# Kernel tuning notes

Hardware: AMD Instinct MI355X
Metric: run time of the kernel (lower is better)

Reference implementation:

```python
import jax, jax.numpy as jnp
import numpy as np

B, L, D, H, NL, DFF = 32, 64, 256, 8, 2, 2048
S, I, DSEM, DDENSE, DSPARSE = 16, 16, 128, 128, 128


def layer_norm(x, g, b, eps=1e-5):
    m = x.mean(-1, keepdims=True)
    v = ((x - m) ** 2).mean(-1, keepdims=True)
    return (x - m) / jnp.sqrt(v + eps) * g + b


def encoder_layer(x, ipw, ipb, ow, ob, g1, b1, g2, b2, f1w, f1b, f2w, f2b):
    # PyTorch TransformerEncoderLayer (post-norm, ReLU FFN, dropout inactive).
    b, t, d = x.shape
    dh = d // H
    qkv = x @ ipw.T + ipb  # (b,t,3d)
    q, k, v = jnp.split(qkv, 3, axis=-1)
    split_heads = lambda z: z.reshape(b, t, H, dh).transpose(0, 2, 1, 3)
    q, k, v = split_heads(q), split_heads(k), split_heads(v)
    att = jax.nn.softmax(jnp.einsum('bhqd,bhkd->bhqk', q, k) / np.float32(np.sqrt(dh)), axis=-1)
    o = jnp.einsum('bhqk,bhkd->bhqd', att, v).transpose(0, 2, 1, 3).reshape(b, t, d)
    x = layer_norm(x + o @ ow.T + ob, g1, b1)
    h = jax.nn.relu(x @ f1w.T + f1b) @ f2w.T + f2b
    return layer_norm(x + h, g2, b2)


def setup_inputs() -> dict:
    key = jax.random.key(0)
    ks = jax.random.split(key, 16)
    sc = np.float32(0.02)
    return dict(
        dense=jax.random.normal(ks[0], (B, L, DDENSE), jnp.float32),
        sparse=jax.random.normal(ks[1], (B, L, DSPARSE), jnp.float32),
        W_feat=jax.random.normal(ks[2], (DDENSE + DSPARSE, D), jnp.float32) * sc,
        b_feat=jnp.zeros((D,), jnp.float32),
        in_proj_w=jax.random.normal(ks[3], (NL, 3 * D, D), jnp.float32) * sc,
        in_proj_b=jnp.zeros((NL, 3 * D), jnp.float32),
        out_w=jax.random.normal(ks[4], (NL, D, D), jnp.float32) * sc,
        out_b=jnp.zeros((NL, D), jnp.float32),
        ln1_g=jnp.ones((NL, D), jnp.float32), ln1_b=jnp.zeros((NL, D), jnp.float32),
        ln2_g=jnp.ones((NL, D), jnp.float32), ln2_b=jnp.zeros((NL, D), jnp.float32),
        ff1_w=jax.random.normal(ks[5], (NL, DFF, D), jnp.float32) * sc,
        ff1_b=jnp.zeros((NL, DFF), jnp.float32),
        ff2_w=jax.random.normal(ks[6], (NL, D, DFF), jnp.float32) * sc,
        ff2_b=jnp.zeros((NL, D), jnp.float32),
        w_act=jax.random.normal(ks[7], (D, 1), jnp.float32) * sc,
        w_route_ws=jax.random.normal(ks[8], (L, S, D), jnp.float32) * sc,
        w_pose_ws=jax.random.normal(ks[9], (L, S, D, D), jnp.float32) * sc,
        w_route_si=jax.random.normal(ks[10], (S, I, D), jnp.float32) * sc,
        w_pose_si=jax.random.normal(ks[11], (S, I, D, D), jnp.float32) * sc,
        cls_w=jax.random.normal(ks[12], (DSEM, 2 * D), jnp.float32) * sc,
        cls_b=jnp.zeros((DSEM,), jnp.float32),
        inorm_g=jnp.ones((DSEM,), jnp.float32),
        inorm_b=jnp.zeros((DSEM,), jnp.float32),
    )


def reference(dense, sparse, W_feat, b_feat, in_proj_w, in_proj_b, out_w, out_b,
              ln1_g, ln1_b, ln2_g, ln2_b, ff1_w, ff1_b, ff2_w, ff2_b,
              w_act, w_route_ws, w_pose_ws, w_route_si, w_pose_si,
              cls_w, cls_b, inorm_g, inorm_b):
    # TokenFeaturizer: concat(dense, sparse) -> Linear -> (b,L,d)
    tok = jnp.concatenate([dense, sparse], axis=-1) @ W_feat + b_feat
    cls = tok.sum(axis=1, keepdims=True)  # einsum 'bld->bd' CLS token
    x = jnp.concatenate([tok, cls], axis=1)  # (b, L+1, d)
    for i in range(in_proj_w.shape[0]):
        x = encoder_layer(x, in_proj_w[i], in_proj_b[i], out_w[i], out_b[i],
                          ln1_g[i], ln1_b[i], ln2_g[i], ln2_b[i],
                          ff1_w[i], ff1_b[i], ff2_w[i], ff2_b[i])
    words, cls_tok = x[:, :L], x[:, L]  # (b,L,d), (b,d)

    # --- route words -> slots ('weighted_sig') ---
    a_words = jax.nn.sigmoid((words @ w_act)[..., 0])  # (b,L)
    c_ws = jax.nn.softmax(jnp.einsum('lsd,bld->bls', w_route_ws, words), axis=-1)
    a_num = jnp.einsum('bls,bl->bs', c_ws, a_words)
    a_slots = a_num / a_words.sum(axis=1, keepdims=True)
    u_hat = jnp.einsum('lsij,blj->blsi', w_pose_ws, words)  # (b,L,S,d)
    u_num = jnp.einsum('bls,bl,blsi->bsi', c_ws, a_words, u_hat)
    u_slots = u_num / a_num[..., None]  # (b,S,d)

    # --- route slots -> intents ---
    c_si = jax.nn.softmax(jnp.einsum('sid,bsd->bsi', w_route_si, u_slots), axis=-1)
    an = jnp.einsum('bsi,bs->bi', c_si, a_slots)
    a_intents = an / (a_slots.sum(axis=1, keepdims=True) + 1e-8)
    u_hat_i = jnp.einsum('sijk,bsk->bsik', w_pose_si, u_slots)  # (b,S,I,d)
    un = jnp.einsum('bsi,bs,bsik->bik', c_si, a_slots, u_hat_i)
    u_intents = un / (an[..., None] + 1e-8)  # (b,I,d)

    # argmax over intents, gather winning pose
    idx = jnp.argmax(a_intents, axis=-1)  # (b,)
    poses = u_intents[jnp.arange(u_intents.shape[0]), idx]  # (b,d)
    intents = jnp.concatenate([cls_tok, poses], axis=-1) @ cls_w.T + cls_b
    intents = layer_norm(intents, inorm_g, inorm_b)
    return (c_ws, intents)
```

## Files before the change

### kernel.cpp

```cpp
#include <hip/hip_runtime.h>
#include <hip/hip_bf16.h>
#include <math.h>

#define B_ 32
#define L_ 64
#define D_ 256
#define H_ 8
#define T_ 65
#define NT_ (B_*T_)
#define DFF_ 2048
#define S_ 16
#define I_ 16
#define DSEM_ 128

typedef __attribute__((ext_vector_type(8))) short bf16x8;
typedef __attribute__((ext_vector_type(4))) float f32x4;

typedef __attribute__((address_space(1))) const void gbl_void;
typedef __attribute__((address_space(3))) void lds_void;
#define GLOAD16(g, l) __builtin_amdgcn_global_load_lds((gbl_void*)(g), (lds_void*)(l), 16, 0, 0)

__device__ inline unsigned short f2bu(float f) {
  union { float f; unsigned u; } a; a.f = f;
  unsigned r = a.u + 0x7FFF + ((a.u >> 16) & 1);
  return (unsigned short)(r >> 16);
}
__device__ inline float b2f(unsigned short u) {
  union { unsigned u; float f; } a; a.u = ((unsigned)u) << 16;
  return a.f;
}

__device__ inline float wave_reduce_sum(float v) {
#pragma unroll
  for (int m = 32; m >= 1; m >>= 1) v += __shfl_xor(v, m, 64);
  return v;
}

__device__ inline float block_reduce_sum_256(float v, float* sred) {
  v = wave_reduce_sum(v);
  int tid = threadIdx.x;
  if ((tid & 63) == 0) sred[tid >> 6] = v;
  __syncthreads();
  float r = sred[0] + sred[1] + sred[2] + sred[3];
  __syncthreads();
  return r;
}

__global__ __launch_bounds__(256) void conv_fused_kernel(
    const float* __restrict__ dense, const float* __restrict__ sparse, unsigned short* __restrict__ cat,
    const float* __restrict__ wfeat, unsigned short* __restrict__ wfeatT,
    const float* __restrict__ ipw, const float* __restrict__ ow,
    const float* __restrict__ f1w, const float* __restrict__ f2w,
    unsigned short* __restrict__ ipwB, unsigned short* __restrict__ owB,
    unsigned short* __restrict__ f1wB, unsigned short* __restrict__ f2wB) {
  __shared__ float tb[64][65];
  int bid = blockIdx.x, tid = threadIdx.x;
  if (bid < 2048) {
    int idx = bid * 256 + tid;
    int r = idx >> 8, c = idx & 255;
    float v = (c < 128) ? dense[r * 128 + c] : sparse[r * 128 + (c - 128)];
    cat[idx] = f2bu(v);
  } else if (bid < 2064) {
    int blk = bid - 2048;
    int k0 = (blk & 3) * 64, n0 = (blk >> 2) * 64;
    int wid = tid >> 6, lane = tid & 63;
#pragma unroll
    for (int p = 0; p < 16; ++p)
      tb[p * 4 + wid][lane] = wfeat[(size_t)(k0 + p * 4 + wid) * 256 + n0 + lane];
    __syncthreads();
#pragma unroll
    for (int p = 0; p < 16; ++p)
      wfeatT[(size_t)(n0 + p * 4 + wid) * 256 + k0 + lane] = f2bu(tb[lane][p * 4 + wid]);
  } else {
    int i = (bid - 2064) * 256 + tid;
    const float* src; unsigned short* dst; int off;
    if (i < 98304)       { src = ipw; dst = ipwB; off = i; }
    else if (i < 131072) { src = ow;  dst = owB;  off = i - 98304; }
    else if (i < 393216) { src = f1w; dst = f1wB; off = i - 131072; }
    else                 { src = f2w; dst = f2wB; off = i - 393216; }
    float4 v = ((const float4*)src)[off];
    short4 o;
    o.x = (short)f2bu(v.x); o.y = (short)f2bu(v.y);
    o.z = (short)f2bu(v.z); o.w = (short)f2bu(v.w);
    ((short4*)dst)[off] = o;
  }
}

template <int ACT, int OUT_BF16, int NFRAG>
__global__ __launch_bounds__(256) void gemm_bf2_kernel(const unsigned short* __restrict__ A,
                                                       const unsigned short* __restrict__ W,
                                                       const float* __restrict__ bias,
                                                       float* __restrict__ Cf, unsigned short* __restrict__ Cb,
                                                       int M, int N, int K) {
  __shared__ __align__(16) unsigned short As[2][32 * 64];
  __shared__ __align__(16) unsigned short Bs[2][NFRAG * 64 * 64];
  int tid = threadIdx.x, wid = tid >> 6, lane = tid & 63;
  int row0 = blockIdx.y * 32, col0 = blockIdx.x * (64 * NFRAG);
  int lr = lane >> 3;
  int sc = ((lane & 7) ^ (lr & 7)) << 3;
  const unsigned short* Asrc = A + (size_t)(row0 + wid * 8 + lr) * K + sc;
  const unsigned short* Bsrc[2 * NFRAG];
#pragma unroll
  for (int p = 0; p < 2 * NFRAG; ++p)
    Bsrc[p] = W + (size_t)(col0 + wid * 16 * NFRAG + p * 8 + lr) * K + sc;
  unsigned short* AsW = &As[0][0] + wid * (8 * 64);
  unsigned short* BsW = &Bs[0][0] + wid * (16 * NFRAG * 64);

  f32x4 acc[2][NFRAG];
#pragma unroll
  for (int i = 0; i < 2; ++i)
#pragma unroll
    for (int j = 0; j < NFRAG; ++j) acc[i][j] = (f32x4){0.f, 0.f, 0.f, 0.f};

  GLOAD16(Asrc, AsW);
#pragma unroll
  for (int p = 0; p < 2 * NFRAG; ++p) GLOAD16(Bsrc[p], BsW + p * (8 * 64));

  int nk = K >> 6, cur = 0;
  int kg = lane >> 4, l15 = lane & 15;
  for (int kt = 0; kt < nk; ++kt) {
    __syncthreads();
    if (kt + 1 < nk) {
      int k0 = (kt + 1) << 6;
      GLOAD16(Asrc + k0, AsW + (cur ^ 1) * (32 * 64));
#pragma unroll
      for (int p = 0; p < 2 * NFRAG; ++p)
        GLOAD16(Bsrc[p] + k0, BsW + (cur ^ 1) * (NFRAG * 64 * 64) + p * (8 * 64));
    }
    const unsigned short* Ab = &As[cur][0];
    const unsigned short* Bb = &Bs[cur][0];
#pragma unroll
    for (int kk = 0; kk < 2; ++kk) {
      int cc = kk * 4 + kg;
      bf16x8 bfr[NFRAG];
#pragma unroll
      for (int fn = 0; fn < NFRAG; ++fn) {
        int rn = wid * 16 * NFRAG + fn * 16 + l15;
        bfr[fn] = *(const bf16x8*)&Bb[rn * 64 + ((cc ^ (rn & 7)) << 3)];
      }
#pragma unroll
      for (int fm = 0; fm < 2; ++fm) {
        int rm = fm * 16 + l15;
        bf16x8 afr = *(const bf16x8*)&Ab[rm * 64 + ((cc ^ (rm & 7)) << 3)];
#pragma unroll
        for (int fn = 0; fn < NFRAG; ++fn)
          acc[fm][fn] = __builtin_amdgcn_mfma_f32_16x16x32_bf16(afr, bfr[fn], acc[fm][fn], 0, 0, 0);
      }
    }
    cur ^= 1;
  }
#pragma unroll
  for (int fm = 0; fm < 2; ++fm) {
#pragma unroll
    for (int fn = 0; fn < NFRAG; ++fn) {
      int col = col0 + wid * 16 * NFRAG + fn * 16 + l15;
      float bi = bias[col];
      int rbase = row0 + fm * 16 + ((lane >> 4) << 2);
#pragma unroll
      for (int r = 0; r < 4; ++r) {
        int grow = rbase + r;
        float v = acc[fm][fn][r] + bi;
        if (ACT == 1) v = fmaxf(v, 0.f);
        if (OUT_BF16) Cb[(size_t)grow * N + col] = f2bu(v);
        else          Cf[(size_t)grow * N + col] = v;
      }
    }
  }
}

__global__ __launch_bounds__(256) void gemm_ln_kernel(const unsigned short* __restrict__ A,
                                                      const unsigned short* __restrict__ W,
                                                      const float* __restrict__ bias,
                                                      const float* __restrict__ gw, const float* __restrict__ gb,
                                                      float* X, unsigned short* __restrict__ xbf,
                                                      int K) {
  __shared__ __align__(16) unsigned short As[2][32 * 64];
  __shared__ __align__(16) unsigned short Bs[2][4 * 64 * 64];
  __shared__ float sred[4][32], sredq[4][32];
  int tid = threadIdx.x, wid = tid >> 6, lane = tid & 63;
  int row0 = blockIdx.y * 32;
  int lr = lane >> 3;
  int sc = ((lane & 7) ^ (lr & 7)) << 3;
  const unsigned short* Asrc = A + (size_t)(row0 + wid * 8 + lr) * K + sc;
  const unsigned short* Bsrc[8];
#pragma unroll
  for (int p = 0; p < 8; ++p)
    Bsrc[p] = W + (size_t)(wid * 64 + p * 8 + lr) * K + sc;
  unsigned short* AsW = &As[0][0] + wid * (8 * 64);
  unsigned short* BsW = &Bs[0][0] + wid * (64 * 64);

  f32x4 acc[2][4];
#pragma unroll
  for (int i = 0; i < 2; ++i)
#pragma unroll
    for (int j = 0; j < 4; ++j) acc[i][j] = (f32x4){0.f, 0.f, 0.f, 0.f};

  GLOAD16(Asrc, AsW);
#pragma unroll
  for (int p = 0; p < 8; ++p) GLOAD16(Bsrc[p], BsW + p * (8 * 64));

  int nk = K >> 6, cur = 0;
  int kg = lane >> 4, l15 = lane & 15;
  for (int kt = 0; kt < nk; ++kt) {
    __syncthreads();
    if (kt + 1 < nk) {
      int k0 = (kt + 1) << 6;
      GLOAD16(Asrc + k0, AsW + (cur ^ 1) * (32 * 64));
#pragma unroll
      for (int p = 0; p < 8; ++p)
        GLOAD16(Bsrc[p] + k0, BsW + (cur ^ 1) * (4 * 64 * 64) + p * (8 * 64));
    }
    const unsigned short* Ab = &As[cur][0];
    const unsigned short* Bb = &Bs[cur][0];
#pragma unroll
    for (int kk = 0; kk < 2; ++kk) {
      int cc = kk * 4 + kg;
      bf16x8 bfr[4];
#pragma unroll
      for (int fn = 0; fn < 4; ++fn) {
        int rn = wid * 64 + fn * 16 + l15;
        bfr[fn] = *(const bf16x8*)&Bb[rn * 64 + ((cc ^ (rn & 7)) << 3)];
      }
#pragma unroll
      for (int fm = 0; fm < 2; ++fm) {
        int rm = fm * 16 + l15;
        bf16x8 afr = *(const bf16x8*)&Ab[rm * 64 + ((cc ^ (rm & 7)) << 3)];
#pragma unroll
        for (int fn = 0; fn < 4; ++fn)
          acc[fm][fn] = __builtin_amdgcn_mfma_f32_16x16x32_bf16(afr, bfr[fn], acc[fm][fn], 0, 0, 0);
      }
    }
    cur ^= 1;
  }
  int g = lane >> 4;
  float v[2][4][4];
  float rs[2][4], rq[2][4];
#pragma unroll
  for (int fm = 0; fm < 2; ++fm)
#pragma unroll
    for (int r = 0; r < 4; ++r) { rs[fm][r] = 0.f; rq[fm][r] = 0.f; }
#pragma unroll
  for (int fm = 0; fm < 2; ++fm) {
    int grow0 = row0 + fm * 16 + g * 4;
#pragma unroll
    for (int fn = 0; fn < 4; ++fn) {
      int col = wid * 64 + fn * 16 + l15;
      float bi = bias[col];
#pragma unroll
      for (int r = 0; r < 4; ++r) {
        float val = acc[fm][fn][r] + bi + X[(size_t)(grow0 + r) * 256 + col];
        v[fm][fn][r] = val;
        rs[fm][r] += val;
        rq[fm][r] += val * val;
      }
    }
  }
#pragma unroll
  for (int m = 1; m <= 8; m <<= 1) {
#pragma unroll
    for (int fm = 0; fm < 2; ++fm)
#pragma unroll
      for (int r = 0; r < 4; ++r) {
        rs[fm][r] += __shfl_xor(rs[fm][r], m, 64);
        rq[fm][r] += __shfl_xor(rq[fm][r], m, 64);
      }
  }
  if (l15 == 0) {
#pragma unroll
    for (int fm = 0; fm < 2; ++fm)
#pragma unroll
      for (int r = 0; r < 4; ++r) {
        int row = fm * 16 + g * 4 + r;
        sred[wid][row] = rs[fm][r];
        sredq[wid][row] = rq[fm][r];
      }
  }
  __syncthreads();
#pragma unroll
  for (int fm = 0; fm < 2; ++fm) {
#pragma unroll
    for (int r = 0; r < 4; ++r) {
      int row = fm * 16 + g * 4 + r;
      float tsum = sred[0][row] + sred[1][row] + sred[2][row] + sred[3][row];
      float tsq = sredq[0][row] + sredq[1][row] + sredq[2][row] + sredq[3][row];
      float mean = tsum * (1.f / 256.f);
      float var = tsq * (1.f / 256.f) - mean * mean;
      float rstd = 1.f / sqrtf(var + 1e-5f);
      int grow = row0 + row;
#pragma unroll
      for (int fn = 0; fn < 4; ++fn) {
        int col = wid * 64 + fn * 16 + l15;
        float o = (v[fm][fn][r] - mean) * rstd * gw[col] + gb[col];
        X[(size_t)grow * 256 + col] = o;
        xbf[(size_t)grow * 256 + col] = f2bu(o);
      }
    }
  }
}

__global__ void build_x_kernel(const float* __restrict__ tok, float* __restrict__ x,
                               unsigned short* __restrict__ xbf) {
  int b = blockIdx.x, d = threadIdx.x;
  float s = 0.f;
  for (int l = 0; l < L_; ++l) {
    float v = tok[((size_t)(b * L_ + l)) * D_ + d];
    size_t o = ((size_t)(b * T_ + l)) * D_ + d;
    x[o] = v; xbf[o] = f2bu(v);
    s += v;
  }
  size_t o = ((size_t)(b * T_ + L_)) * D_ + d;
  x[o] = s; xbf[o] = f2bu(s);
}

__global__ __launch_bounds__(256) void attn_kernel(const unsigned short* __restrict__ qkv,
                                                   unsigned short* __restrict__ attn_out) {
  int bh = blockIdx.x;
  int b = bh >> 3, h = bh & 7;
  __shared__ float Q[T_][32], K[T_][32], V[T_][32];
  __shared__ float Sc[T_][T_ + 1];
  int tid = threadIdx.x;
  for (int idx = tid; idx < T_ * 32; idx += 256) {
    int t = idx >> 5, d = idx & 31;
    const unsigned short* base = qkv + ((size_t)(b * T_ + t)) * 768 + h * 32 + d;
    Q[t][d] = b2f(base[0]);
    K[t][d] = b2f(base[256]);
    V[t][d] = b2f(base[512]);
  }
  __syncthreads();
  for (int idx = tid; idx < T_ * T_; idx += 256) {
    int qi = idx / T_, ki = idx % T_;
    float s = 0.f;
#pragma unroll
    for (int d = 0; d < 32; ++d) s += Q[qi][d] * K[ki][d];
    Sc[qi][ki] = s * 0.17677669529663687f;
  }
  __syncthreads();
  {
    int q = tid & 3;
    for (int row = tid >> 2; row < T_; row += 64) {
      float mx = -1e30f;
      for (int k = q; k < T_; k += 4) mx = fmaxf(mx, Sc[row][k]);
      mx = fmaxf(mx, __shfl_xor(mx, 1, 64));
      mx = fmaxf(mx, __shfl_xor(mx, 2, 64));
      float sum = 0.f;
      for (int k = q; k < T_; k += 4) { float e = expf(Sc[row][k] - mx); Sc[row][k] = e; sum += e; }
      sum += __shfl_xor(sum, 1, 64);
      sum += __shfl_xor(sum, 2, 64);
      float inv = 1.f / sum;
      for (int k = q; k < T_; k += 4) Sc[row][k] *= inv;
    }
  }
  __syncthreads();
  for (int idx = tid; idx < T_ * 32; idx += 256) {
    int t = idx >> 5, d = idx & 31;
    float acc = 0.f;
    for (int k = 0; k < T_; ++k) acc += Sc[t][k] * V[k][d];
    attn_out[((size_t)(b * T_ + t)) * D_ + h * 32 + d] = f2bu(acc);
  }
}

__global__ __launch_bounds__(256) void cws_kernel(const float* __restrict__ x, const float* __restrict__ w_route,
                                                  const float* __restrict__ w_act, float* __restrict__ c_ws_out,
                                                  float* __restrict__ a_words) {
  int bl = blockIdx.x;
  int b = bl >> 6, l = bl & 63;
  __shared__ float word[256];
  __shared__ float logits[16];
  __shared__ float sred[4];
  int t = threadIdx.x;
  word[t] = x[((size_t)(b * T_ + l)) * D_ + t];
  __syncthreads();
  float pa = word[t] * w_act[t];
  float asum = block_reduce_sum_256(pa, sred);
  if (t == 0) a_words[b * 64 + l] = 1.f / (1.f + expf(-asum));
  int s = t >> 4, j0 = t & 15;
  float p = 0.f;
  for (int j = j0; j < 256; j += 16) p += w_route[((size_t)(l * 16 + s)) * 256 + j] * word[j];
#pragma unroll
  for (int m = 8; m >= 1; m >>= 1) p += __shfl_xor(p, m, 64);
  if (j0 == 0) logits[s] = p;
  __syncthreads();
  if (t < 16) {
    float mx = -1e30f;
#pragma unroll
    for (int k = 0; k < 16; ++k) mx = fmaxf(mx, logits[k]);
    float sum = 0.f;
#pragma unroll
    for (int k = 0; k < 16; ++k) sum += expf(logits[k] - mx);
    c_ws_out[(size_t)bl * 16 + t] = expf(logits[t] - mx) / sum;
  }
}

__global__ __launch_bounds__(64) void slot_agg_kernel(const float* __restrict__ c_ws, const float* __restrict__ a_words,
                                                      float* __restrict__ a_num, float* __restrict__ a_slots,
                                                      float* __restrict__ asl_sum) {
  int b = blockIdx.x, lane = threadIdx.x;
  float aw = a_words[b * 64 + lane];
  float asum = wave_reduce_sum(aw);
  float inv = 1.f / asum;
  float ssum = 0.f;
  for (int s = 0; s < 16; ++s) {
    float p = c_ws[((size_t)(b * 64 + lane)) * 16 + s] * aw;
    float r = wave_reduce_sum(p);
    if (lane == 0) {
      a_num[b * 16 + s] = r;
      a_slots[b * 16 + s] = r * inv;
      ssum += r * inv;
    }
  }
  if (lane == 0) asl_sum[b] = ssum;
}

__global__ __launch_bounds__(256, 4) void pose_ws3_kernel(const unsigned short* __restrict__ xbf,
                                                          const float* __restrict__ P,
                                                          const float* __restrict__ c_ws,
                                                          const float* __restrict__ a_words,
                                                          float* __restrict__ partial) {
  int bid = blockIdx.x;
  int ih = bid & 1, s = (bid >> 1) & 15, lg = bid >> 5;
  int iBase = ih * 128;
  __shared__ __align__(16) unsigned short Bs[32 * 256];
  int tid = threadIdx.x, wid = tid >> 6, lane = tid & 63;
  int kg = lane >> 4, l15 = lane & 15;
  f32x4 acc[2][2];
#pragma unroll
  for (int i = 0; i < 2; ++i)
#pragma unroll
    for (int j = 0; j < 2; ++j) acc[i][j] = (f32x4){0.f, 0.f, 0.f, 0.f};

#pragma unroll
  for (int li = 0; li < 2; ++li) {
    int l = lg + li * 32;
    __syncthreads();
    {
      int b = tid >> 3, c0 = (tid & 7) * 4;
      float w = c_ws[((size_t)(b * 64 + l)) * 16 + s] * a_words[b * 64 + l];
      const unsigned short* src = xbf + ((size_t)(b * T_ + l)) * D_;
#pragma unroll
      for (int j = 0; j < 4; ++j) {
        int c = c0 + j;
        union { float4 f4; unsigned short u[8]; } in, out;
        in.f4 = *(const float4*)(src + c * 8);
#pragma unroll
        for (int e = 0; e < 8; ++e) out.u[e] = f2bu(w * b2f(in.u[e]));
        *(float4*)&Bs[b * 256 + ((c ^ (b & 7)) << 3)] = out.f4;
      }
    }
    __syncthreads();
    const float* Pbase = P + (((size_t)(l * 16 + s)) << 16);
#pragma unroll
    for (int k0 = 0; k0 < 256; k0 += 64) {
#pragma unroll
      for (int kk = 0; kk < 2; ++kk) {
        int cc = (k0 >> 3) + kk * 4 + kg;
        bf16x8 bfr[2];
#pragma unroll
        for (int fn = 0; fn < 2; ++fn) {
          int rb = fn * 16 + l15;
          bfr[fn] = *(const bf16x8*)&Bs[rb * 256 + ((cc ^ (rb & 7)) << 3)];
        }
        int kbase = k0 + kk * 32 + kg * 8;
#pragma unroll
        for (int fm = 0; fm < 2; ++fm) {
          int row = iBase + wid * 32 + fm * 16 + l15;
          const float* src = Pbase + (size_t)row * 256 + kbase;
          float4 v0 = *(const float4*)src;
          float4 v1 = *(const float4*)(src + 4);
          union { bf16x8 b8; unsigned short u[8]; } pk;
          pk.u[0] = f2bu(v0.x); pk.u[1] = f2bu(v0.y); pk.u[2] = f2bu(v0.z); pk.u[3] = f2bu(v0.w);
          pk.u[4] = f2bu(v1.x); pk.u[5] = f2bu(v1.y); pk.u[6] = f2bu(v1.z); pk.u[7] = f2bu(v1.w);
          acc[fm][0] = __builtin_amdgcn_mfma_f32_16x16x32_bf16(pk.b8, bfr[0], acc[fm][0], 0, 0, 0);
          acc[fm][1] = __builtin_amdgcn_mfma_f32_16x16x32_bf16(pk.b8, bfr[1], acc[fm][1], 0, 0, 0);
        }
      }
    }
  }
  float* pout = partial + ((size_t)(lg * 16 + s)) * 8192;
#pragma unroll
  for (int fm = 0; fm < 2; ++fm) {
#pragma unroll
    for (int fn = 0; fn < 2; ++fn) {
      int b = fn * 16 + l15;
      int i0 = iBase + wid * 32 + fm * 16 + (kg << 2);
#pragma unroll
      for (int r = 0; r < 4; ++r)
        pout[(i0 + r) * 32 + b] = acc[fm][fn][r];
    }
  }
}

__global__ __launch_bounds__(256) void reduce_uslots_kernel(const float* __restrict__ partial,
                                                            const float* __restrict__ a_num,
                                                            float* __restrict__ u_slots) {
  int s = blockIdx.x >> 5, ic = blockIdx.x & 31;
  int t = threadIdx.x;
  int i = ic * 8 + (t >> 5), b = t & 31;
  size_t off = (size_t)s * 8192 + i * 32 + b;
  float a0 = 0.f, a1 = 0.f, a2 = 0.f, a3 = 0.f;
#pragma unroll
  for (int lg = 0; lg < 32; lg += 4) {
    a0 += partial[((size_t)(lg + 0) * 16) * 8192 + off];
    a1 += partial[((size_t)(lg + 1) * 16) * 8192 + off];
    a2 += partial[((size_t)(lg + 2) * 16) * 8192 + off];
    a3 += partial[((size_t)(lg + 3) * 16) * 8192 + off];
  }
  u_slots[((size_t)(b * 16 + s)) * 256 + i] = (a0 + a1 + a2 + a3) / a_num[b * 16 + s];
}

__global__ __launch_bounds__(256) void csi_kernel(const float* __restrict__ u_slots, const float* __restrict__ w_route_si,
                                                  float* __restrict__ c_si) {
  int bs = blockIdx.x;
  int s = bs & 15;
  __shared__ float row[256];
  __shared__ float logits[16];
  int t = threadIdx.x;
  row[t] = u_slots[(size_t)bs * 256 + t];
  __syncthreads();
  int i = t >> 4, j0 = t & 15;
  float p = 0.f;
  for (int j = j0; j < 256; j += 16) p += w_route_si[((size_t)(s * 16 + i)) * 256 + j] * row[j];
#pragma unroll
  for (int m = 8; m >= 1; m >>= 1) p += __shfl_xor(p, m, 64);
  if (j0 == 0) logits[i] = p;
  __syncthreads();
  if (t < 16) {
    float mx = -1e30f;
#pragma unroll
    for (int k = 0; k < 16; ++k) mx = fmaxf(mx, logits[k]);
    float sum = 0.f;
#pragma unroll
    for (int k = 0; k < 16; ++k) sum += expf(logits[k] - mx);
    c_si[(size_t)bs * 16 + t] = expf(logits[t] - mx) / sum;
  }
}

__global__ void pose_si_partial_kernel(const float* __restrict__ P, float* __restrict__ R4) {
  int si = blockIdx.x >> 2, jc = blockIdx.x & 3;
  int k = threadIdx.x;
  const float* base = P + (size_t)si * 65536 + (size_t)jc * 64 * 256 + k;
  float a0 = 0.f, a1 = 0.f, a2 = 0.f, a3 = 0.f;
#pragma unroll
  for (int j = 0; j < 64; j += 4) {
    a0 += base[(j + 0) * 256];
    a1 += base[(j + 1) * 256];
    a2 += base[(j + 2) * 256];
    a3 += base[(j + 3) * 256];
  }
  R4[(size_t)jc * 65536 + si * 256 + k] = a0 + a1 + a2 + a3;
}

__global__ __launch_bounds__(256) void un_merged_kernel(const float* __restrict__ c_si,
                                                        const float* __restrict__ a_slots,
                                                        const float* __restrict__ R4,
                                                        const float* __restrict__ u_slots,
                                                        float* __restrict__ u_pose) {
  int b = blockIdx.x, t = threadIdx.x;
  __shared__ float csi_s[256];
  __shared__ float asl_s[16];
  __shared__ float an_s[16];
  __shared__ float w_s[16];
  __shared__ float an_star;
  __shared__ int istar_s;
  csi_s[t] = c_si[(size_t)b * 256 + t];
  if (t < 16) asl_s[t] = a_slots[b * 16 + t];
  __syncthreads();
  if (t < 16) {
    float acc = 0.f;
#pragma unroll
    for (int s = 0; s < 16; ++s) acc += csi_s[s * 16 + t] * asl_s[s];
    an_s[t] = acc;
  }
  __syncthreads();
  if (t == 0) {
    int best = 0;
    float bv = an_s[0];
    for (int k = 1; k < 16; ++k)
      if (an_s[k] > bv) { bv = an_s[k]; best = k; }
    istar_s = best;
    an_star = bv;
  }
  __syncthreads();
  int istar = istar_s;
  if (t < 16) w_s[t] = csi_s[t * 16 + istar] * asl_s[t];
  __syncthreads();
  float acc = 0.f;
#pragma unroll
  for (int s = 0; s < 16; ++s) {
    size_t ro = ((size_t)(s * 16 + istar)) * 256 + t;
    float r = R4[ro] + R4[65536 + ro] + R4[131072 + ro] + R4[196608 + ro];
    acc += w_s[s] * r * u_slots[((size_t)(b * 16 + s)) * 256 + t];
  }
  u_pose[(size_t)b * 256 + t] = acc / (an_star + 1e-8f);
}

__global__ __launch_bounds__(128) void final_kernel(const float* __restrict__ x, const float* __restrict__ u_pose,
                                                    const float* __restrict__ cls_w,
                                                    const float* __restrict__ cls_b, const float* __restrict__ g,
                                                    const float* __restrict__ bb, float* __restrict__ out) {
  int b = blockIdx.x, m = threadIdx.x;
  __shared__ float row[512];
  __shared__ float sred[2];
  for (int d = m; d < 256; d += 128) {
    row[d] = x[((size_t)(b * T_ + L_)) * D_ + d];
    row[256 + d] = u_pose[(size_t)b * 256 + d];
  }
  __syncthreads();
  float acc = cls_b[m];
  for (int j = 0; j < 512; ++j) acc += cls_w[(size_t)m * 512 + j] * row[j];
  float v = wave_reduce_sum(acc);
  if ((m & 63) == 0) sred[m >> 6] = v;
  __syncthreads();
  float mean = (sred[0] + sred[1]) * (1.f / 128.f);
  __syncthreads();
  float dv = acc - mean;
  float v2 = wave_reduce_sum(dv * dv);
  if ((m & 63) == 0) sred[m >> 6] = v2;
  __syncthreads();
  float var = (sred[0] + sred[1]) * (1.f / 128.f);
  out[(size_t)b * 128 + m] = dv * (1.f / sqrtf(var + 1e-5f)) * g[m] + bb[m];
}

extern "C" void kernel_launch(void* const* d_in, const int* in_sizes, int n_in,
                              void* d_out, int out_size, void* d_ws, size_t ws_size,
                              hipStream_t stream) {
  (void)in_sizes; (void)n_in; (void)out_size; (void)ws_size;
  const float* dense      = (const float*)d_in[0];
  const float* sparse     = (const float*)d_in[1];
  const float* W_feat     = (const float*)d_in[2];
  const float* b_feat     = (const float*)d_in[3];
  const float* in_proj_w  = (const float*)d_in[4];
  const float* in_proj_b  = (const float*)d_in[5];
  const float* out_w      = (const float*)d_in[6];
  const float* out_b      = (const float*)d_in[7];
  const float* ln1_g      = (const float*)d_in[8];
  const float* ln1_b      = (const float*)d_in[9];
  const float* ln2_g      = (const float*)d_in[10];
  const float* ln2_b      = (const float*)d_in[11];
  const float* ff1_w      = (const float*)d_in[12];
  const float* ff1_b      = (const float*)d_in[13];
  const float* ff2_w      = (const float*)d_in[14];
  const float* ff2_b      = (const float*)d_in[15];
  const float* w_act      = (const float*)d_in[16];
  const float* w_route_ws = (const float*)d_in[17];
  const float* w_pose_ws  = (const float*)d_in[18];
  const float* w_route_si = (const float*)d_in[19];
  const float* w_pose_si  = (const float*)d_in[20];
  const float* cls_w      = (const float*)d_in[21];
  const float* cls_b      = (const float*)d_in[22];
  const float* inorm_g    = (const float*)d_in[23];
  const float* inorm_b    = (const float*)d_in[24];

  float* ws = (float*)d_ws;
  float* X       = ws;
  float* PROJ    = X + 532480;
  float* a_words = PROJ + 532480;
  float* a_num   = a_words + 2048;
  float* a_slots = a_num + 512;
  float* asl_sum = a_slots + 512;
  float* u_slots = asl_sum + 32;
  float* c_si    = u_slots + 131072;
  float* u_pose  = c_si + 8192;
  float* R4      = u_pose + 8192;

  unsigned short* bfb   = (unsigned short*)(R4 + 262144);
  unsigned short* Xbf   = bfb;
  unsigned short* QKVbf = Xbf + 532480;
  unsigned short* HAR   = QKVbf + 1597440;
  unsigned short* CATbf = HAR;
  unsigned short* ATTNbf= HAR + 2097152;
  unsigned short* wfeatT= HAR + 4259840;
  unsigned short* ipwB  = wfeatT + 65536;
  unsigned short* owB   = ipwB + 393216;
  unsigned short* f1wB  = owB + 131072;
  unsigned short* f2wB  = f1wB + 1048576;
  float* partial = (float*)QKVbf;

  float* c_ws_out    = (float*)d_out;
  float* intents_out = (float*)d_out + 32768;

  conv_fused_kernel<<<4624, 256, 0, stream>>>(dense, sparse, CATbf, W_feat, wfeatT,
                                              in_proj_w, out_w, ff1_w, ff2_w,
                                              ipwB, owB, f1wB, f2wB);

  gemm_bf2_kernel<0, 0, 1><<<dim3(4, 64), 256, 0, stream>>>(CATbf, wfeatT, b_feat, PROJ, nullptr, 2048, 256, 256);
  build_x_kernel<<<32, 256, 0, stream>>>(PROJ, X, Xbf);

  for (int layer = 0; layer < 2; ++layer) {
    const unsigned short* ipw = ipwB + (size_t)layer * 196608;
    const unsigned short* ow  = owB + (size_t)layer * 65536;
    const unsigned short* f1w = f1wB + (size_t)layer * 524288;
    const unsigned short* f2w = f2wB + (size_t)layer * 524288;
    const float* ipb = in_proj_b + (size_t)layer * 768;
    const float* ob  = out_b + (size_t)layer * 256;
    const float* g1  = ln1_g + (size_t)layer * 256;
    const float* b1  = ln1_b + (size_t)layer * 256;
    const float* g2  = ln2_g + (size_t)layer * 256;
    const float* b2  = ln2_b + (size_t)layer * 256;
    const float* f1b = ff1_b + (size_t)layer * DFF_;
    const float* f2b = ff2_b + (size_t)layer * 256;

    gemm_bf2_kernel<0, 1, 2><<<dim3(6, 65), 256, 0, stream>>>(Xbf, ipw, ipb, nullptr, QKVbf, NT_, 768, 256);
    attn_kernel<<<B_ * H_, 256, 0, stream>>>(QKVbf, ATTNbf);
    gemm_ln_kernel<<<dim3(1, 65), 256, 0, stream>>>(ATTNbf, ow, ob, g1, b1, X, Xbf, 256);
    gemm_bf2_kernel<1, 1, 2><<<dim3(16, 65), 256, 0, stream>>>(Xbf, f1w, f1b, nullptr, HAR, NT_, DFF_, 256);
    gemm_ln_kernel<<<dim3(1, 65), 256, 0, stream>>>(HAR, f2w, f2b, g2, b2, X, Xbf, 2048);
  }

  cws_kernel<<<2048, 256, 0, stream>>>(X, w_route_ws, w_act, c_ws_out, a_words);
  slot_agg_kernel<<<32, 64, 0, stream>>>(c_ws_out, a_words, a_num, a_slots, asl_sum);
  pose_ws3_kernel<<<1024, 256, 0, stream>>>(Xbf, w_pose_ws, c_ws_out, a_words, partial);
  reduce_uslots_kernel<<<512, 256, 0, stream>>>(partial, a_num, u_slots);
  pose_si_partial_kernel<<<1024, 256, 0, stream>>>(w_pose_si, R4);
  csi_kernel<<<512, 256, 0, stream>>>(u_slots, w_route_si, c_si);
  un_merged_kernel<<<32, 256, 0, stream>>>(c_si, a_slots, R4, u_slots, u_pose);
  final_kernel<<<32, 128, 0, stream>>>(X, u_pose, cls_w, cls_b, inorm_g, inorm_b, intents_out);
}
```

Measured before the change: 299.3 us.

## Unfuse GEMM+LayerNorm into generic GEMM plus separate residual-LN kernel

Replaces the fused GEMM+residual+LayerNorm kernel, which ran only 65 blocks each covering all 256 output columns, with the generic bf16 GEMM over a 4x65 grid writing fp32 to a scratch buffer. A separate per-row residual-add LayerNorm kernel follows. The aim is four times more blocks for the out-projection and FFN2 GEMMs, especially the K=2048 one, so the GPU is better occupied. The cost is two extra launches per layer and an fp32 round trip through global memory for the projection output.

```diff
diff --git a/kernel.cpp b/kernel.cpp
--- a/kernel.cpp
+++ b/kernel.cpp
@@ -168,134 +168,18 @@
   }
 }
 
-__global__ __launch_bounds__(256) void gemm_ln_kernel(const unsigned short* __restrict__ A,
-                                                      const unsigned short* __restrict__ W,
-                                                      const float* __restrict__ bias,
-                                                      const float* __restrict__ gw, const float* __restrict__ gb,
-                                                      float* X, unsigned short* __restrict__ xbf,
-                                                      int K) {
-  __shared__ __align__(16) unsigned short As[2][32 * 64];
-  __shared__ __align__(16) unsigned short Bs[2][4 * 64 * 64];
-  __shared__ float sred[4][32], sredq[4][32];
-  int tid = threadIdx.x, wid = tid >> 6, lane = tid & 63;
-  int row0 = blockIdx.y * 32;
-  int lr = lane >> 3;
-  int sc = ((lane & 7) ^ (lr & 7)) << 3;
-  const unsigned short* Asrc = A + (size_t)(row0 + wid * 8 + lr) * K + sc;
-  const unsigned short* Bsrc[8];
-#pragma unroll
-  for (int p = 0; p < 8; ++p)
-    Bsrc[p] = W + (size_t)(wid * 64 + p * 8 + lr) * K + sc;
-  unsigned short* AsW = &As[0][0] + wid * (8 * 64);
-  unsigned short* BsW = &Bs[0][0] + wid * (64 * 64);
-
-  f32x4 acc[2][4];
-#pragma unroll
-  for (int i = 0; i < 2; ++i)
-#pragma unroll
-    for (int j = 0; j < 4; ++j) acc[i][j] = (f32x4){0.f, 0.f, 0.f, 0.f};
-
-  GLOAD16(Asrc, AsW);
-#pragma unroll
-  for (int p = 0; p < 8; ++p) GLOAD16(Bsrc[p], BsW + p * (8 * 64));
-
-  int nk = K >> 6, cur = 0;
-  int kg = lane >> 4, l15 = lane & 15;
-  for (int kt = 0; kt < nk; ++kt) {
-    __syncthreads();
-    if (kt + 1 < nk) {
-      int k0 = (kt + 1) << 6;
-      GLOAD16(Asrc + k0, AsW + (cur ^ 1) * (32 * 64));
-#pragma unroll
-      for (int p = 0; p < 8; ++p)
-        GLOAD16(Bsrc[p] + k0, BsW + (cur ^ 1) * (4 * 64 * 64) + p * (8 * 64));
-    }
-    const unsigned short* Ab = &As[cur][0];
-    const unsigned short* Bb = &Bs[cur][0];
-#pragma unroll
-    for (int kk = 0; kk < 2; ++kk) {
-      int cc = kk * 4 + kg;
-      bf16x8 bfr[4];
-#pragma unroll
-      for (int fn = 0; fn < 4; ++fn) {
-        int rn = wid * 64 + fn * 16 + l15;
-        bfr[fn] = *(const bf16x8*)&Bb[rn * 64 + ((cc ^ (rn & 7)) << 3)];
-      }
-#pragma unroll
-      for (int fm = 0; fm < 2; ++fm) {
-        int rm = fm * 16 + l15;
-        bf16x8 afr = *(const bf16x8*)&Ab[rm * 64 + ((cc ^ (rm & 7)) << 3)];
-#pragma unroll
-        for (int fn = 0; fn < 4; ++fn)
-          acc[fm][fn] = __builtin_amdgcn_mfma_f32_16x16x32_bf16(afr, bfr[fn], acc[fm][fn], 0, 0, 0);
-      }
-    }
-    cur ^= 1;
-  }
-  int g = lane >> 4;
-  float v[2][4][4];
-  float rs[2][4], rq[2][4];
-#pragma unroll
-  for (int fm = 0; fm < 2; ++fm)
-#pragma unroll
-    for (int r = 0; r < 4; ++r) { rs[fm][r] = 0.f; rq[fm][r] = 0.f; }
-#pragma unroll
-  for (int fm = 0; fm < 2; ++fm) {
-    int grow0 = row0 + fm * 16 + g * 4;
-#pragma unroll
-    for (int fn = 0; fn < 4; ++fn) {
-      int col = wid * 64 + fn * 16 + l15;
-      float bi = bias[col];
-#pragma unroll
-      for (int r = 0; r < 4; ++r) {
-        float val = acc[fm][fn][r] + bi + X[(size_t)(grow0 + r) * 256 + col];
-        v[fm][fn][r] = val;
-        rs[fm][r] += val;
-        rq[fm][r] += val * val;
-      }
-    }
-  }
-#pragma unroll
-  for (int m = 1; m <= 8; m <<= 1) {
-#pragma unroll
-    for (int fm = 0; fm < 2; ++fm)
-#pragma unroll
-      for (int r = 0; r < 4; ++r) {
-        rs[fm][r] += __shfl_xor(rs[fm][r], m, 64);
-        rq[fm][r] += __shfl_xor(rq[fm][r], m, 64);
-      }
-  }
-  if (l15 == 0) {
-#pragma unroll
-    for (int fm = 0; fm < 2; ++fm)
-#pragma unroll
-      for (int r = 0; r < 4; ++r) {
-        int row = fm * 16 + g * 4 + r;
-        sred[wid][row] = rs[fm][r];
-        sredq[wid][row] = rq[fm][r];
-      }
-  }
-  __syncthreads();
-#pragma unroll
-  for (int fm = 0; fm < 2; ++fm) {
-#pragma unroll
-    for (int r = 0; r < 4; ++r) {
-      int row = fm * 16 + g * 4 + r;
-      float tsum = sred[0][row] + sred[1][row] + sred[2][row] + sred[3][row];
-      float tsq = sredq[0][row] + sredq[1][row] + sredq[2][row] + sredq[3][row];
-      float mean = tsum * (1.f / 256.f);
-      float var = tsq * (1.f / 256.f) - mean * mean;
-      float rstd = 1.f / sqrtf(var + 1e-5f);
-      int grow = row0 + row;
-#pragma unroll
-      for (int fn = 0; fn < 4; ++fn) {
-        int col = wid * 64 + fn * 16 + l15;
-        float o = (v[fm][fn][r] - mean) * rstd * gw[col] + gb[col];
-        X[(size_t)grow * 256 + col] = o;
-        xbf[(size_t)grow * 256 + col] = f2bu(o);
-      }
-    }
-  }
+__global__ __launch_bounds__(256) void ln_residual_kernel(float* __restrict__ x, unsigned short* __restrict__ xbf,
+                                                          const float* __restrict__ proj,
+                                                          const float* __restrict__ g, const float* __restrict__ bb) {
+  __shared__ float sred[4];
+  int r = blockIdx.x, d = threadIdx.x;
+  float v = x[(size_t)r * D_ + d] + proj[(size_t)r * D_ + d];
+  float mean = block_reduce_sum_256(v, sred) * (1.f / 256.f);
+  float dv = v - mean;
+  float var = block_reduce_sum_256(dv * dv, sred) * (1.f / 256.f);
+  float o = dv * (1.f / sqrtf(var + 1e-5f)) * g[d] + bb[d];
+  x[(size_t)r * D_ + d] = o;
+  xbf[(size_t)r * D_ + d] = f2bu(o);
 }
 
 __global__ void build_x_kernel(const float* __restrict__ tok, float* __restrict__ x,
@@ -701,9 +585,11 @@
 
     gemm_bf2_kernel<0, 1, 2><<<dim3(6, 65), 256, 0, stream>>>(Xbf, ipw, ipb, nullptr, QKVbf, NT_, 768, 256);
     attn_kernel<<<B_ * H_, 256, 0, stream>>>(QKVbf, ATTNbf);
-    gemm_ln_kernel<<<dim3(1, 65), 256, 0, stream>>>(ATTNbf, ow, ob, g1, b1, X, Xbf, 256);
+    gemm_bf2_kernel<0, 0, 1><<<dim3(4, 65), 256, 0, stream>>>(ATTNbf, ow, ob, PROJ, nullptr, NT_, 256, 256);
+    ln_residual_kernel<<<NT_, 256, 0, stream>>>(X, Xbf, PROJ, g1, b1);
     gemm_bf2_kernel<1, 1, 2><<<dim3(16, 65), 256, 0, stream>>>(Xbf, f1w, f1b, nullptr, HAR, NT_, DFF_, 256);
-    gemm_ln_kernel<<<dim3(1, 65), 256, 0, stream>>>(HAR, f2w, f2b, g2, b2, X, Xbf, 2048);
+    gemm_bf2_kernel<0, 0, 1><<<dim3(4, 65), 256, 0, stream>>>(HAR, f2w, f2b, PROJ, nullptr, NT_, 256, 2048);
+    ln_residual_kernel<<<NT_, 256, 0, stream>>>(X, Xbf, PROJ, g2, b2);
   }
 
   cws_kernel<<<2048, 256, 0, stream>>>(X, w_route_ws, w_act, c_ws_out, a_words);
```

Measured after the change: 279.3 us. 1.07x faster.
